# Performance work log

Measured on AMD Instinct MI355X. Metric: run time of the kernel, lower is better.

Reference implementation:

```python
import jax, jax.numpy as jnp
import numpy as np

N, R, D, T, H, MM, OBJ, PLN = 1024, 100, 256, 14, 8, 600, 36, 16
DH = D // H


def _plin(w, x):
    # monotone piecewise-linear map on [0,1] with PLN segments (Counter's PiecewiseLin)
    w = jnp.abs(w).at[0].set(0.0)
    w = w / w.sum()
    cs = jnp.cumsum(w)  # knot values, cs[PLN] == 1
    y = PLN * jnp.clip(x, 0.0, 1.0)
    i = jnp.clip(jnp.floor(y).astype(jnp.int32), 0, PLN)
    f = y - jnp.floor(y)
    return cs[i] + f * w[jnp.clip(i + 1, 0, PLN)]


def _iou(b):
    # b: (N, m, 4) as x1,y1,x2,y2 -> pairwise IoU (N, m, m)
    area = jnp.clip(b[..., 2] - b[..., 0], 0.0) * jnp.clip(b[..., 3] - b[..., 1], 0.0)
    lt = jnp.maximum(b[:, :, None, :2], b[:, None, :, :2])
    rb = jnp.minimum(b[:, :, None, 2:], b[:, None, :, 2:])
    wh = jnp.clip(rb - lt, 0.0)
    inter = wh[..., 0] * wh[..., 1]
    return inter / (area[:, :, None] + area[:, None, :] - inter + 1e-12)


def _counter(boxes, att, pw):
    # Zhang et al. counting module, already_sigmoided=True
    att_top, idx = jax.lax.top_k(att, OBJ)                       # (N, m)
    btop = jnp.take_along_axis(boxes, idx[:, :, None], axis=1)   # (N, m, 4)
    rel = att_top[:, :, None] * att_top[:, None, :]              # outer product of attention
    dist = 1.0 - _iou(btop)
    score = _plin(pw[0], rel) * _plin(pw[1], dist)
    dscore = _plin(pw[3], rel) * _plin(pw[4], dist)
    # deduplication via outer differences
    att_diff = jnp.abs(att_top[:, :, None] - att_top[:, None, :])
    sd = jnp.abs(dscore[:, :, :, None] - dscore[:, :, None, :])  # (N, m, m, m)
    sim = jnp.prod(_plin(pw[2], 1.0 - sd), axis=1) * _plin(pw[2], 1.0 - att_diff)
    row_sims = sim.sum(axis=2)                                   # (N, m), >= 1 (diagonal)
    all_sims = row_sims[:, :, None] * row_sims[:, None, :]
    score = score / all_sims
    correction = _plin(pw[0], att_top * att_top) / row_sims
    total = jnp.sqrt(score.sum(axis=(1, 2)) + correction.sum(axis=1) + 1e-20)  # (N,)
    # to_one_hot: soft one-hot between floor and ceil counts
    s = jnp.clip(total, 0.0, float(OBJ))
    i = jnp.clip(jnp.floor(s).astype(jnp.int32), 0, OBJ)
    f = s - jnp.floor(s)
    oh_l = jax.nn.one_hot(i, OBJ + 1, dtype=s.dtype)
    oh_r = jax.nn.one_hot(jnp.clip(i + 1, 0, OBJ), OBJ + 1, dtype=s.dtype)
    one_hot = (1.0 - f)[:, None] * oh_l + f[:, None] * oh_r
    att_conf = jnp.abs(_plin(pw[5], att_top) - 0.5)
    dist_conf = jnp.abs(_plin(pw[6], dist) - 0.5)
    conf = _plin(pw[7], att_conf.mean(axis=1) + dist_conf.mean(axis=(1, 2)))  # (N,)
    return one_hot * conf[:, None], conf


def _layernorm(x, g, b):
    mu = x.mean(-1, keepdims=True)
    var = ((x - mu) ** 2).mean(-1, keepdims=True)
    return (x - mu) / jnp.sqrt(var + 1e-5) * g + b


def setup_inputs():
    key = jax.random.key(0)
    ks = jax.random.split(key, 20)
    lin = lambda k, o, i: jax.random.normal(k, (o, i), dtype=jnp.float32) * 0.02
    z = lambda o: jnp.zeros((o,), jnp.float32)
    v_emb = jax.random.normal(ks[0], (N, R, D), dtype=jnp.float32)
    q_emb = jax.random.normal(ks[1], (N, T, D), dtype=jnp.float32)
    xy = jax.random.uniform(ks[2], (N, R, 2), dtype=jnp.float32) * 0.8
    wh = jax.random.uniform(ks[3], (N, R, 2), dtype=jnp.float32) * 0.19 + 0.01
    boxes = jnp.concatenate([xy, xy + wh], axis=-1)  # valid x1,y1,x2,y2 in [0,1]
    pw = jax.random.uniform(ks[4], (8, PLN + 1), dtype=jnp.float32, minval=0.5, maxval=1.5)
    pw = pw.at[:, 0].set(0.0)
    return {
        'v_emb': v_emb, 'q_emb': q_emb, 'boxes': boxes,
        'Wq': lin(ks[5], D, D), 'bq': z(D),
        'Wk': lin(ks[6], D, D), 'bk': z(D),
        'Wv': lin(ks[7], D, D), 'bv': z(D),
        'in_w': lin(ks[8], 3 * D, D), 'in_b': z(3 * D),
        'out_w': lin(ks[9], D, D), 'out_b': z(D),
        'ln_g': jnp.ones((D,), jnp.float32), 'ln_b': z(D),
        'l0_w': lin(ks[10], MM, D), 'l0_b': z(MM),
        'l1_w': lin(ks[11], MM, D), 'l1_b': z(MM),
        'lo_w': lin(ks[12], 1, MM), 'lo_b': z(1),
        'pw': pw,
    }


def reference(v_emb, q_emb, boxes, Wq, bq, Wk, bk, Wv, bv, in_w, in_b, out_w, out_b,
              ln_g, ln_b, l0_w, l0_b, l1_w, l1_b, lo_w, lo_b, pw):
    n = v_emb.shape[0]
    # pre-projections then nn.MultiheadAttention (eval, no dropout)
    q = v_emb @ Wq.T + bq
    k = v_emb @ Wk.T + bk
    v = v_emb @ Wv.T + bv
    wq, wk, wv = jnp.split(in_w, 3, axis=0)
    biq, bik, biv = jnp.split(in_b, 3)
    qh = (q @ wq.T + biq).reshape(n, R, H, DH)
    kh = (k @ wk.T + bik).reshape(n, R, H, DH)
    vh = (v @ wv.T + biv).reshape(n, R, H, DH)
    logits = jnp.einsum('nqhd,nkhd->nhqk', qh, kh) * (1.0 / np.sqrt(DH))
    attn = jax.nn.softmax(logits, axis=-1)
    ao = jnp.einsum('nhqk,nkhd->nqhd', attn, vh).reshape(n, R, D)
    ao = ao @ out_w.T + out_b
    inter = _layernorm(ao, ln_g, ln_b)
    # MLB bilinear fusion with mean-pooled question, normalize=True, no activations
    q_pool = q_emb.mean(axis=1)                 # (N, D)
    x0 = inter @ l0_w.T + l0_b                  # (N, R, MM)
    x1 = q_pool @ l1_w.T + l1_b                 # (N, MM)
    zf = x0 * x1[:, None, :]
    zf = jnp.sign(zf) * jnp.sqrt(jnp.abs(zf))   # signed sqrt
    zf = zf / jnp.maximum(jnp.linalg.norm(zf, axis=-1, keepdims=True), 1e-12)
    scores = jax.nn.sigmoid(zf @ lo_w.T + lo_b)  # (N, R, 1)
    pred, conf = _counter(boxes, scores[..., 0], pw)
    return scores, pred, conf
```

## Files before the change

### kernel.cpp

```cpp
#include <hip/hip_runtime.h>

#define N_   1024
#define R_   100
#define D_   256
#define T_   14
#define H_   8
#define DH_  32
#define MM_  600
#define OBJ_ 36

typedef _Float16 f16;
typedef __attribute__((ext_vector_type(8))) _Float16 f16x8;
typedef __attribute__((ext_vector_type(4))) _Float16 f16x4v;
typedef __attribute__((ext_vector_type(4))) float f32x4;

__device__ __forceinline__ void f2h_split(float x, f16& hi, f16& lo) {
  hi = (_Float16)x;
  lo = (_Float16)(x - (float)hi);
}

#define GL16(gp, lp) __builtin_amdgcn_global_load_lds( \
    (const __attribute__((address_space(1))) void*)(gp), \
    (__attribute__((address_space(3))) void*)(lp), 16, 0, 0)

__device__ __forceinline__ float plin_f(const float* __restrict__ w,
                                        const float* __restrict__ cs, float x) {
  float xc = fminf(fmaxf(x, 0.f), 1.f);
  float y  = 16.f * xc;
  float fy = floorf(y);
  int   i  = (int)fy;
  float f  = y - fy;
  int   ip = i + 1; if (ip > 16) ip = 16;
  return cs[i] + f * w[ip];
}

__global__ void prep_plin(const float* __restrict__ pw, float* __restrict__ plw,
                          float* __restrict__ plc) {
  int p = threadIdx.x;
  if (p < 8) {
    float w[17];
    float sum = 0.f;
    w[0] = 0.f;
    for (int k = 1; k < 17; ++k) { w[k] = fabsf(pw[p*17 + k]); sum += w[k]; }
    float inv = 1.f / sum;
    float c = 0.f;
    for (int k = 0; k < 17; ++k) {
      float wk = w[k] * inv;
      c += wk;
      plw[p*17 + k] = wk;
      plc[p*17 + k] = c;
    }
  }
}

__global__ void fuse_c(const float* __restrict__ in_w, const float* __restrict__ in_b,
                       const float* __restrict__ bq, const float* __restrict__ bk,
                       const float* __restrict__ bv, float* __restrict__ c) {
  int i = blockIdx.x * blockDim.x + threadIdx.x;
  if (i < 768) {
    const float* bsel = (i < 256) ? bq : ((i < 512) ? bk : bv);
    float acc = in_b[i];
    for (int o = 0; o < 256; ++o) acc += in_w[(size_t)i*256 + o] * bsel[o];
    c[i] = acc;
  }
}

__global__ __launch_bounds__(256) void fuse_A(const float* __restrict__ in_w,
    const float* __restrict__ Wq, const float* __restrict__ Wk,
    const float* __restrict__ Wv, f16* __restrict__ Ahi, f16* __restrict__ Alo) {
  int i = blockIdx.x;
  int j = threadIdx.x;
  const float* Wsel = (i < 256) ? Wq : ((i < 512) ? Wk : Wv);
  __shared__ float row[256];
  row[j] = in_w[(size_t)i*256 + j];
  __syncthreads();
  float acc = 0.f;
  for (int o = 0; o < 256; ++o) acc += row[o] * Wsel[(size_t)o*256 + j];
  f16 h, l; f2h_split(acc, h, l);
  Ahi[(size_t)i*256 + j] = h;
  Alo[(size_t)i*256 + j] = l;
}

__global__ __launch_bounds__(256) void split_vec(const float* __restrict__ in,
    f16* __restrict__ hi, f16* __restrict__ lo, int n4) {
  int i = blockIdx.x * blockDim.x + threadIdx.x;
  if (i < n4) {
    float4 v = ((const float4*)in)[i];
    union { f16 h[4]; ushort4 u; } H, L;
    f2h_split(v.x, H.h[0], L.h[0]);
    f2h_split(v.y, H.h[1], L.h[1]);
    f2h_split(v.z, H.h[2], L.h[2]);
    f2h_split(v.w, H.h[3], L.h[3]);
    ((ushort4*)hi)[i] = H.u;
    ((ushort4*)lo)[i] = L.u;
  }
}

__global__ __launch_bounds__(256) void conv_w600(const float* __restrict__ w,
    f16* __restrict__ hi, f16* __restrict__ lo) {
  int o = blockIdx.x;
  int j = threadIdx.x;
  f16 h = (f16)0.f, l = (f16)0.f;
  if (o < 600) f2h_split(w[(size_t)o*256 + j], h, l);
  hi[(size_t)o*256 + j] = h;
  lo[(size_t)o*256 + j] = l;
}

__global__ __launch_bounds__(256) void pool_split(const float* __restrict__ q_emb,
    f16* __restrict__ qph, f16* __restrict__ qpl) {
  int n = blockIdx.x, tid = threadIdx.x;
  float s = 0.f;
  for (int t = 0; t < 14; ++t) s += q_emb[((size_t)n*14 + t)*256 + tid];
  s *= (1.f/14.f);
  f16 h, l; f2h_split(s, h, l);
  qph[(size_t)n*256 + tid] = h;
  qpl[(size_t)n*256 + tid] = l;
}

template<bool BOUND>
__global__ __launch_bounds__(256) void gemm_f16s(
    const f16* __restrict__ Xhi, const f16* __restrict__ Xlo,
    const f16* __restrict__ Whi, const f16* __restrict__ Wlo,
    const float* __restrict__ bias, float* __restrict__ C, int Oreal) {
  __shared__ f16 XsH[128 * 32];
  __shared__ f16 XsL[128 * 32];
  __shared__ f16 WsH[128 * 32];
  __shared__ f16 WsL[128 * 32];
  const int tid  = threadIdx.x;
  const int wave = tid >> 6, lane = tid & 63;
  const int bm = blockIdx.x * 128, bn = blockIdx.y * 128;
  const int wm = (wave & 1) * 64, wn = (wave >> 1) * 64;
  const int col = lane & 15, quad = lane >> 4;

  const int s = wave * 64 + lane;
  const int r0 = s >> 2,         cseg = (s & 3) * 8;
  const int r1 = (s + 256) >> 2;
  const size_t o0 = (size_t)(bm + r0) * 256 + cseg;
  const size_t o1 = (size_t)(bm + r1) * 256 + cseg;
  const size_t p0 = (size_t)(bn + r0) * 256 + cseg;
  const size_t p1 = (size_t)(bn + r1) * 256 + cseg;
  char* XHB = (char*)XsH + wave * 1024;
  char* XLB = (char*)XsL + wave * 1024;
  char* WHB = (char*)WsH + wave * 1024;
  char* WLB = (char*)WsL + wave * 1024;

  f32x4 acc[4][4] = {};

  for (int k0 = 0; k0 < 256; k0 += 32) {
    GL16(Xhi + o0 + k0, XHB);
    GL16(Xhi + o1 + k0, XHB + 4096);
    GL16(Xlo + o0 + k0, XLB);
    GL16(Xlo + o1 + k0, XLB + 4096);
    GL16(Whi + p0 + k0, WHB);
    GL16(Whi + p1 + k0, WHB + 4096);
    GL16(Wlo + p0 + k0, WLB);
    GL16(Wlo + p1 + k0, WLB + 4096);
    __syncthreads();

    f16x8 ah[4], al[4], bh[4], bl[4];
#pragma unroll
    for (int i = 0; i < 4; ++i) {
      int ro = (wm + i*16 + col) * 32 + quad * 8;
      ah[i] = *(const f16x8*)(XsH + ro);
      al[i] = *(const f16x8*)(XsL + ro);
    }
#pragma unroll
    for (int j = 0; j < 4; ++j) {
      int ro = (wn + j*16 + col) * 32 + quad * 8;
      bh[j] = *(const f16x8*)(WsH + ro);
      bl[j] = *(const f16x8*)(WsL + ro);
    }
#pragma unroll
    for (int i = 0; i < 4; ++i)
#pragma unroll
      for (int j = 0; j < 4; ++j) {
        acc[i][j] = __builtin_amdgcn_mfma_f32_16x16x32_f16(al[i], bh[j], acc[i][j], 0, 0, 0);
        acc[i][j] = __builtin_amdgcn_mfma_f32_16x16x32_f16(ah[i], bl[j], acc[i][j], 0, 0, 0);
        acc[i][j] = __builtin_amdgcn_mfma_f32_16x16x32_f16(ah[i], bh[j], acc[i][j], 0, 0, 0);
      }
    __syncthreads();
  }

#pragma unroll
  for (int j = 0; j < 4; ++j) {
    int o = bn + wn + j*16 + col;
    if (BOUND && o >= Oreal) continue;
    float bo = bias[o];
#pragma unroll
    for (int i = 0; i < 4; ++i) {
#pragma unroll
      for (int r = 0; r < 4; ++r) {
        int m = bm + wm + i*16 + quad*4 + r;
        C[(size_t)m * Oreal + o] = acc[i][j][r] + bo;
      }
    }
  }
}

__global__ __launch_bounds__(256) void gemm2_ln(
    const f16* __restrict__ Xhi, const f16* __restrict__ Xlo,
    const f16* __restrict__ Whi, const f16* __restrict__ Wlo,
    const float* __restrict__ bias, const float* __restrict__ g,
    const float* __restrict__ b, f16* __restrict__ ohi, f16* __restrict__ olo) {
  __shared__ f16 XsH[128 * 32];
  __shared__ f16 XsL[128 * 32];
  __shared__ f16 WsH[256 * 32];
  __shared__ f16 WsL[256 * 32];
  __shared__ float gbb[768];
  const int tid  = threadIdx.x;
  const int wave = tid >> 6, lane = tid & 63;
  const int bm = blockIdx.x * 128;
  const int wm = wave * 32;
  const int col16 = lane & 15, quad = lane >> 4;

  for (int i = tid; i < 768; i += 256)
    gbb[i] = (i < 256) ? g[i] : ((i < 512) ? b[i - 256] : bias[i - 512]);

  const int s = wave * 64 + lane;
  const int rx0 = s >> 2, cseg = (s & 3) * 8;
  const int rx1 = (s + 256) >> 2;
  const size_t o0 = (size_t)(bm + rx0) * 256 + cseg;
  const size_t o1 = (size_t)(bm + rx1) * 256 + cseg;
  char* XHB = (char*)XsH + wave * 1024;
  char* XLB = (char*)XsL + wave * 1024;

  f32x4 acc[2][16] = {};

  for (int k0 = 0; k0 < 256; k0 += 32) {
    GL16(Xhi + o0 + k0, XHB);
    GL16(Xhi + o1 + k0, XHB + 4096);
    GL16(Xlo + o0 + k0, XLB);
    GL16(Xlo + o1 + k0, XLB + 4096);
#pragma unroll
    for (int is = 0; is < 4; ++is) {
      int sw = is * 256 + s;
      size_t wo = (size_t)(sw >> 2) * 256 + (sw & 3) * 8 + k0;
      GL16(Whi + wo, (char*)WsH + is * 4096 + wave * 1024);
      GL16(Wlo + wo, (char*)WsL + is * 4096 + wave * 1024);
    }
    __syncthreads();

    f16x8 ah[2], al[2];
#pragma unroll
    for (int i = 0; i < 2; ++i) {
      int ro = (wm + i*16 + col16) * 32 + quad * 8;
      ah[i] = *(const f16x8*)(XsH + ro);
      al[i] = *(const f16x8*)(XsL + ro);
    }
#pragma unroll
    for (int j = 0; j < 16; ++j) {
      int ro = (j*16 + col16) * 32 + quad * 8;
      f16x8 bh = *(const f16x8*)(WsH + ro);
      f16x8 bl = *(const f16x8*)(WsL + ro);
#pragma unroll
      for (int i = 0; i < 2; ++i) {
        acc[i][j] = __builtin_amdgcn_mfma_f32_16x16x32_f16(al[i], bh, acc[i][j], 0, 0, 0);
        acc[i][j] = __builtin_amdgcn_mfma_f32_16x16x32_f16(ah[i], bl, acc[i][j], 0, 0, 0);
        acc[i][j] = __builtin_amdgcn_mfma_f32_16x16x32_f16(ah[i], bh, acc[i][j], 0, 0, 0);
      }
    }
    __syncthreads();
  }

#pragma unroll
  for (int i = 0; i < 2; ++i) {
#pragma unroll
    for (int r = 0; r < 4; ++r) {
      float x[16];
      float sum = 0.f;
#pragma unroll
      for (int j = 0; j < 16; ++j) {
        float v = acc[i][j][r] + gbb[512 + j*16 + col16];
        x[j] = v;
        sum += v;
      }
#pragma unroll
      for (int msk = 1; msk < 16; msk <<= 1) sum += __shfl_xor(sum, msk, 64);
      float mu = sum * (1.f/256.f);
      float s2 = 0.f;
#pragma unroll
      for (int j = 0; j < 16; ++j) { float d = x[j] - mu; s2 += d * d; }
#pragma unroll
      for (int msk = 1; msk < 16; msk <<= 1) s2 += __shfl_xor(s2, msk, 64);
      float inv = rsqrtf(s2 * (1.f/256.f) + 1e-5f);
      size_t m = (size_t)(bm + wm + i*16 + quad*4 + r);
#pragma unroll
      for (int j = 0; j < 16; ++j) {
        int col = j*16 + col16;
        float yv = (x[j] - mu) * inv * gbb[col] + gbb[256 + col];
        f16 hh, ll; f2h_split(yv, hh, ll);
        ohi[m*256 + col] = hh;
        olo[m*256 + col] = ll;
      }
    }
  }
}

__global__ __launch_bounds__(512) void attn_mfma(const float* __restrict__ qkv,
    f16* __restrict__ aohi, f16* __restrict__ aolo) {
  const int n = blockIdx.x >> 3;
  const int h = blockIdx.x & 7;
  __shared__ f16 KH[112*32], KL[112*32];
  __shared__ f16 VTH[32*116], VTL[32*116];
  __shared__ unsigned int P32[112*116];
  const int tid = threadIdx.x;
  const int wave = tid >> 6, lane = tid & 63;
  const int col16 = lane & 15, quad = lane >> 4;
  const float scale = 0.17677669529663687f;
  const float* base = qkv + (size_t)n * 100 * 768 + h * 32;
  const int tm = wave;

  float qv[8];
  if (tm < 7) {
    int m = tm*16 + col16; if (m > 99) m = 99;
    const float* qp = base + (size_t)m * 768 + quad*8;
    float4 q0 = *(const float4*)(qp);
    float4 q1 = *(const float4*)(qp + 4);
    qv[0]=q0.x; qv[1]=q0.y; qv[2]=q0.z; qv[3]=q0.w;
    qv[4]=q1.x; qv[5]=q1.y; qv[6]=q1.z; qv[7]=q1.w;
  } else {
#pragma unroll
    for (int j = 0; j < 8; ++j) qv[j] = 0.f;
  }

  for (int idx = tid; idx < 112*32; idx += 512) {
    int r = idx >> 5, d = idx & 31;
    float kv = 0.f, vv = 0.f;
    if (r < 100) {
      const float* p = base + (size_t)r * 768;
      kv = p[256 + d];
      vv = p[512 + d];
    }
    f16 khh, kll, vhh, vll;
    f2h_split(kv, khh, kll);
    f2h_split(vv, vhh, vll);
    KH[idx] = khh; KL[idx] = kll;
    VTH[d*116 + r] = vhh; VTL[d*116 + r] = vll;
  }
  __syncthreads();

  if (tm < 7) {
    f16x8 ah, al;
#pragma unroll
    for (int j = 0; j < 8; ++j) {
      f16 hh, ll; f2h_split(qv[j] * scale, hh, ll); ah[j] = hh; al[j] = ll;
    }
    f32x4 sacc[7];
#pragma unroll
    for (int tn = 0; tn < 7; ++tn) {
      int off = (tn*16 + col16)*32 + quad*8;
      f16x8 bh = *(const f16x8*)(KH + off);
      f16x8 bl = *(const f16x8*)(KL + off);
      f32x4 a = {};
      a = __builtin_amdgcn_mfma_f32_16x16x32_f16(al, bh, a, 0, 0, 0);
      a = __builtin_amdgcn_mfma_f32_16x16x32_f16(ah, bl, a, 0, 0, 0);
      a = __builtin_amdgcn_mfma_f32_16x16x32_f16(ah, bh, a, 0, 0, 0);
      sacc[tn] = a;
    }
    if (col16 >= 4) {
      sacc[6][0] = -1e30f; sacc[6][1] = -1e30f;
      sacc[6][2] = -1e30f; sacc[6][3] = -1e30f;
    }
    float mx[4];
#pragma unroll
    for (int r = 0; r < 4; ++r) {
      float mv = sacc[0][r];
#pragma unroll
      for (int tn = 1; tn < 7; ++tn) mv = fmaxf(mv, sacc[tn][r]);
      mx[r] = mv;
    }
#pragma unroll
    for (int msk = 1; msk < 16; msk <<= 1)
#pragma unroll
      for (int r = 0; r < 4; ++r) mx[r] = fmaxf(mx[r], __shfl_xor(mx[r], msk, 64));
    float sm[4] = {0.f, 0.f, 0.f, 0.f};
#pragma unroll
    for (int tn = 0; tn < 7; ++tn)
#pragma unroll
      for (int r = 0; r < 4; ++r) {
        float p = __expf(sacc[tn][r] - mx[r]);
        sacc[tn][r] = p;
        sm[r] += p;
      }
#pragma unroll
    for (int msk = 1; msk < 16; msk <<= 1)
#pragma unroll
      for (int r = 0; r < 4; ++r) sm[r] += __shfl_xor(sm[r], msk, 64);
    float inv[4];
#pragma unroll
    for (int r = 0; r < 4; ++r) inv[r] = 1.f / sm[r];
#pragma unroll
    for (int tn = 0; tn < 7; ++tn)
#pragma unroll
      for (int r = 0; r < 4; ++r) {
        float p = sacc[tn][r] * inv[r];
        f16 hh, ll; f2h_split(p, hh, ll);
        union { struct { f16 h, l; } f; unsigned int u; } pk;
        pk.f.h = hh; pk.f.l = ll;
        P32[(tm*16 + quad*4 + r)*116 + tn*16 + col16] = pk.u;
      }

    f16x8 vh[2][4], vl[2][4];
#pragma unroll
    for (int td = 0; td < 2; ++td)
#pragma unroll
      for (int kc = 0; kc < 4; ++kc) {
        if (kc == 3 && quad >= 2) {
          f16x8 z = {};
          vh[td][kc] = z; vl[td][kc] = z;
        } else {
          int off = (td*16 + col16)*116 + kc*32 + quad*8;
          f16x4v h0 = *(const f16x4v*)(VTH + off);
          f16x4v h1 = *(const f16x4v*)(VTH + off + 4);
          f16x4v l0 = *(const f16x4v*)(VTL + off);
          f16x4v l1 = *(const f16x4v*)(VTL + off + 4);
          f16x8 hv, lv;
#pragma unroll
          for (int t = 0; t < 4; ++t) { hv[t] = h0[t]; hv[t+4] = h1[t]; lv[t] = l0[t]; lv[t+4] = l1[t]; }
          vh[td][kc] = hv; vl[td][kc] = lv;
        }
      }
    f32x4 acc[2] = {};
#pragma unroll
    for (int kc = 0; kc < 4; ++kc) {
      f16x8 ph, pl;
      if (kc == 3 && quad >= 2) {
        f16x8 z = {};
        ph = z; pl = z;
      } else {
        const unsigned int* pp = P32 + (tm*16 + col16)*116 + kc*32 + quad*8;
        f16x8 e0 = *(const f16x8*)(pp);
        f16x8 e1 = *(const f16x8*)(pp + 4);
        ph = __builtin_shufflevector(e0, e1, 0, 2, 4, 6, 8, 10, 12, 14);
        pl = __builtin_shufflevector(e0, e1, 1, 3, 5, 7, 9, 11, 13, 15);
      }
#pragma unroll
      for (int td = 0; td < 2; ++td) {
        acc[td] = __builtin_amdgcn_mfma_f32_16x16x32_f16(pl, vh[td][kc], acc[td], 0, 0, 0);
        acc[td] = __builtin_amdgcn_mfma_f32_16x16x32_f16(ph, vl[td][kc], acc[td], 0, 0, 0);
        acc[td] = __builtin_amdgcn_mfma_f32_16x16x32_f16(ph, vh[td][kc], acc[td], 0, 0, 0);
      }
    }
#pragma unroll
    for (int td = 0; td < 2; ++td) {
#pragma unroll
      for (int r = 0; r < 4; ++r) {
        int m = tm*16 + quad*4 + r;
        if (m < 100) {
          size_t oidx = ((size_t)n*100 + m)*256 + h*32 + td*16 + col16;
          f16 hh, ll; f2h_split(acc[td][r], hh, ll);
          aohi[oidx] = hh;
          aolo[oidx] = ll;
        }
      }
    }
  }
}

__global__ __launch_bounds__(256) void mlb_kernel(const float* __restrict__ x0,
    const float* __restrict__ x1, const float* __restrict__ lo_w,
    const float* __restrict__ lo_b, float* __restrict__ out) {
  const int wave = threadIdx.x >> 6, lane = threadIdx.x & 63;
  const size_t m = (size_t)blockIdx.x * 4 + wave;
  const size_t n = m / 100;
  const float* xr = x0 + m * 600;
  const float* yr = x1 + n * 600;
  float ss = 0.f, dot = 0.f;
  for (int e = lane; e < 600; e += 64) {
    float v = xr[e] * yr[e];
    float r = (v >= 0.f) ? sqrtf(v) : -sqrtf(-v);
    ss  += r * r;
    dot += r * lo_w[e];
  }
#pragma unroll
  for (int o = 32; o > 0; o >>= 1) {
    ss  += __shfl_xor(ss, o, 64);
    dot += __shfl_xor(dot, o, 64);
  }
  if (lane == 0) {
    float inv = 1.f / fmaxf(sqrtf(ss), 1e-12f);
    float sc = dot * inv + lo_b[0];
    out[m] = 1.f / (1.f + __expf(-sc));
  }
}

__device__ __forceinline__ float breduce(float v, float* red, int tid) {
  for (int o = 32; o > 0; o >>= 1) v += __shfl_down(v, o, 64);
  if ((tid & 63) == 0) red[tid >> 6] = v;
  __syncthreads();
  float r = red[0] + red[1] + red[2] + red[3];
  __syncthreads();
  return r;
}

__global__ __launch_bounds__(256) void counter_kernel(
    const float* __restrict__ scores, const float* __restrict__ boxes,
    const float* __restrict__ plw, const float* __restrict__ plc,
    float* __restrict__ pred, float* __restrict__ conf_out) {
  int n = blockIdx.x, tid = threadIdx.x;
  __shared__ float plw_s[8][17], plc_s[8][17];
  __shared__ float sval[128];
  __shared__ int   sidx[128];
  __shared__ float att[36], bx[36][4];
  __shared__ float dist[36][36], scr[36][36], ds2[36][36], sim[36][36];
  __shared__ float rs[36];
  __shared__ float red[4];
  __shared__ float b_f, b_cf;
  __shared__ int   b_i;

  for (int i = tid; i < 136; i += 256) {
    (&plw_s[0][0])[i] = plw[i];
    (&plc_s[0][0])[i] = plc[i];
  }
  if (tid < 128) {
    sval[tid] = (tid < 100) ? scores[(size_t)n*100 + tid] : -1e30f;
    sidx[tid] = tid;
  }
  __syncthreads();

  for (int k = 2; k <= 128; k <<= 1) {
    for (int j = k >> 1; j > 0; j >>= 1) {
      if (tid < 128) {
        int ixj = tid ^ j;
        if (ixj > tid) {
          float va = sval[tid], vb = sval[ixj];
          int   ia = sidx[tid], ib = sidx[ixj];
          bool a_before_b = (va > vb) || (va == vb && ia < ib);
          bool ascending = ((tid & k) == 0);
          bool doswap = ascending ? !a_before_b : a_before_b;
          if (doswap) { sval[tid] = vb; sval[ixj] = va; sidx[tid] = ib; sidx[ixj] = ia; }
        }
      }
      __syncthreads();
    }
  }

  if (tid < 36) {
    att[tid] = sval[tid];
    const float* bp = boxes + ((size_t)n*100 + sidx[tid])*4;
    bx[tid][0] = bp[0]; bx[tid][1] = bp[1]; bx[tid][2] = bp[2]; bx[tid][3] = bp[3];
  }
  __syncthreads();

  for (int idx = tid; idx < 1296; idx += 256) {
    int i = idx / 36, j = idx % 36;
    float x1a = bx[i][0], y1a = bx[i][1], x2a = bx[i][2], y2a = bx[i][3];
    float x1b = bx[j][0], y1b = bx[j][1], x2b = bx[j][2], y2b = bx[j][3];
    float areaA = fmaxf(x2a - x1a, 0.f) * fmaxf(y2a - y1a, 0.f);
    float areaB = fmaxf(x2b - x1b, 0.f) * fmaxf(y2b - y1b, 0.f);
    float iw = fmaxf(fminf(x2a, x2b) - fmaxf(x1a, x1b), 0.f);
    float ih = fmaxf(fminf(y2a, y2b) - fmaxf(y1a, y1b), 0.f);
    float inter = iw * ih;
    float iou = inter / (areaA + areaB - inter + 1e-12f);
    float dd = 1.f - iou;
    float rel = att[i] * att[j];
    dist[i][j] = dd;
    scr[i][j]  = plin_f(plw_s[0], plc_s[0], rel) * plin_f(plw_s[1], plc_s[1], dd);
    ds2[i][j]  = plin_f(plw_s[3], plc_s[3], rel) * plin_f(plw_s[4], plc_s[4], dd);
  }
  __syncthreads();

  for (int idx = tid; idx < 1296; idx += 256) {
    int b = idx / 36, c = idx % 36;
    float p = plin_f(plw_s[2], plc_s[2], 1.f - fabsf(att[b] - att[c]));
    for (int a = 0; a < 36; ++a)
      p *= plin_f(plw_s[2], plc_s[2], 1.f - fabsf(ds2[a][b] - ds2[a][c]));
    sim[b][c] = p;
  }
  __syncthreads();

  if (tid < 36) {
    float s = 0.f;
    for (int c = 0; c < 36; ++c) s += sim[tid][c];
    rs[tid] = s;
  }
  __syncthreads();

  float p1 = 0.f, p4 = 0.f;
  for (int idx = tid; idx < 1296; idx += 256) {
    int b = idx / 36, c = idx % 36;
    p1 += scr[b][c] / (rs[b] * rs[c]);
    p4 += fabsf(plin_f(plw_s[6], plc_s[6], dist[b][c]) - 0.5f);
  }
  float p2 = 0.f, p3 = 0.f;
  if (tid < 36) {
    p2 = plin_f(plw_s[0], plc_s[0], att[tid]*att[tid]) / rs[tid];
    p3 = fabsf(plin_f(plw_s[5], plc_s[5], att[tid]) - 0.5f);
  }
  float s1 = breduce(p1, red, tid);
  float s2 = breduce(p2, red, tid);
  float s3 = breduce(p3, red, tid);
  float s4 = breduce(p4, red, tid);

  if (tid == 0) {
    float total = sqrtf(s1 + s2 + 1e-20f);
    float cf = plin_f(plw_s[7], plc_s[7], s3 * (1.f/36.f) + s4 * (1.f/1296.f));
    float sc = fminf(fmaxf(total, 0.f), 36.f);
    float fl = floorf(sc);
    int ii = (int)fl; if (ii > 36) ii = 36;
    b_f = sc - fl;
    b_i = ii;
    b_cf = cf;
    conf_out[n] = cf;
  }
  __syncthreads();
  if (tid < 37) {
    int ii = b_i;
    int ir = (ii + 1 > 36) ? 36 : ii + 1;
    float v = ((tid == ii) ? (1.f - b_f) : 0.f) + ((tid == ir) ? b_f : 0.f);
    pred[(size_t)n*37 + tid] = v * b_cf;
  }
}

extern "C" void kernel_launch(void* const* d_in, const int* in_sizes, int n_in,
                              void* d_out, int out_size, void* d_ws, size_t ws_size,
                              hipStream_t stream) {
  const float* v_emb = (const float*)d_in[0];
  const float* q_emb = (const float*)d_in[1];
  const float* boxes = (const float*)d_in[2];
  const float* Wq    = (const float*)d_in[3];
  const float* bq    = (const float*)d_in[4];
  const float* Wk    = (const float*)d_in[5];
  const float* bk    = (const float*)d_in[6];
  const float* Wv    = (const float*)d_in[7];
  const float* bv    = (const float*)d_in[8];
  const float* in_w  = (const float*)d_in[9];
  const float* in_b  = (const float*)d_in[10];
  const float* out_w = (const float*)d_in[11];
  const float* out_b = (const float*)d_in[12];
  const float* ln_g  = (const float*)d_in[13];
  const float* ln_b  = (const float*)d_in[14];
  const float* l0_w  = (const float*)d_in[15];
  const float* l0_b  = (const float*)d_in[16];
  const float* l1_w  = (const float*)d_in[17];
  const float* l1_b  = (const float*)d_in[18];
  const float* lo_w  = (const float*)d_in[19];
  const float* lo_b  = (const float*)d_in[20];
  const float* pw    = (const float*)d_in[21];

  float* ws = (float*)d_ws;
  float* plw   = ws + 0;
  float* plc   = ws + 256;
  float* cbuf  = ws + 512;
  float* x1    = ws + 1280;
  f16* hb = (f16*)(ws + 615680);
  f16* A_hi    = hb + 0;
  f16* A_lo    = hb + 196608;
  f16* outw_hi = hb + 393216;
  f16* outw_lo = hb + 458752;
  f16* l0w_hi  = hb + 524288;
  f16* l0w_lo  = hb + 688128;
  f16* l1w_hi  = hb + 851968;
  f16* l1w_lo  = hb + 1015808;
  f16* qp_hi   = hb + 1179648;
  f16* qp_lo   = hb + 1441792;
  f16* v_hi    = hb + 1703936;
  f16* v_lo    = hb + 27918336;
  const size_t small_floats = 615680 + 27066368;

  size_t avail = (ws_size / 4 > small_floats) ? (ws_size / 4 - small_floats) : 0;
  int NC = 1024;
  while (NC > 32 && (size_t)NC * 188000ull > avail) NC >>= 1;

  float* qkv_c = ws + small_floats;
  float* x0_c  = qkv_c + (size_t)NC * 76800;
  f16* ao_hi  = (f16*)(x0_c + (size_t)NC * 60000);
  f16* ao_lo  = ao_hi + (size_t)NC * 25600;
  f16* int_hi = ao_lo + (size_t)NC * 25600;
  f16* int_lo = int_hi + (size_t)NC * 25600;

  float* out    = (float*)d_out;
  float* scores = out;
  float* pred   = out + 102400;
  float* conf   = out + 140288;

  prep_plin<<<1, 64, 0, stream>>>(pw, plw, plc);
  fuse_c<<<3, 256, 0, stream>>>(in_w, in_b, bq, bk, bv, cbuf);
  fuse_A<<<768, 256, 0, stream>>>(in_w, Wq, Wk, Wv, A_hi, A_lo);
  split_vec<<<(65536/4 + 255)/256, 256, 0, stream>>>(out_w, outw_hi, outw_lo, 65536/4);
  conv_w600<<<640, 256, 0, stream>>>(l0_w, l0w_hi, l0w_lo);
  conv_w600<<<640, 256, 0, stream>>>(l1_w, l1w_hi, l1w_lo);
  split_vec<<<(26214400/4 + 255)/256, 256, 0, stream>>>(v_emb, v_hi, v_lo, 26214400/4);
  pool_split<<<N_, 256, 0, stream>>>(q_emb, qp_hi, qp_lo);
  {
    dim3 gx(1024/128, 5);
    gemm_f16s<true><<<gx, 256, 0, stream>>>(qp_hi, qp_lo, l1w_hi, l1w_lo,
                                            l1_b, x1, 600);
  }

  for (int n0 = 0; n0 < N_; n0 += NC) {
    const int M = NC * 100;
    const size_t voff = (size_t)n0 * 100 * 256;

    dim3 g1(M / 128, 6);
    gemm_f16s<false><<<g1, 256, 0, stream>>>(v_hi + voff, v_lo + voff,
                                             A_hi, A_lo, cbuf, qkv_c, 768);

    attn_mfma<<<NC * H_, 512, 0, stream>>>(qkv_c, ao_hi, ao_lo);

    gemm2_ln<<<M / 128, 256, 0, stream>>>(ao_hi, ao_lo, outw_hi, outw_lo,
                                          out_b, ln_g, ln_b, int_hi, int_lo);

    dim3 g3(M / 128, 5);
    gemm_f16s<true><<<g3, 256, 0, stream>>>(int_hi, int_lo, l0w_hi, l0w_lo,
                                            l0_b, x0_c, 600);

    mlb_kernel<<<M / 4, 256, 0, stream>>>(x0_c, x1 + (size_t)n0 * 600, lo_w, lo_b,
                                          scores + (size_t)n0 * 100);
  }

  counter_kernel<<<N_, 256, 0, stream>>>(scores, boxes, plw, plc, pred, conf);
}
```

Measured before the change: 988.9 us.

## Fuse MLB signed-sqrt/norm/dot epilogue into l0 GEMM with partial sums

Replaces the l0 GEMM that wrote the full x0 activation (M x 600 floats) plus a separate MLB kernel with a GEMM whose epilogue computes the signed sqrt, the squared norm and the lo_w dot product per row tile. It writes per-tile partial sums, which a small reduce kernel combines into the sigmoid scores. This removes the large x0 write and re-read, and the smaller workspace allows bigger chunks. In exchange it adds shuffle reductions and per-element x1 loads in the epilogue, plus a second small launch.

Measured after the change: 995.6 us. No clear change (+0.7%).

```diff
diff --git a/kernel.cpp b/kernel.cpp
--- a/kernel.cpp
+++ b/kernel.cpp
@@ -197,6 +197,121 @@
   }
 }
 
+__global__ __launch_bounds__(256) void gemm_l0_mlb(
+    const f16* __restrict__ Xhi, const f16* __restrict__ Xlo,
+    const f16* __restrict__ Whi, const f16* __restrict__ Wlo,
+    const float* __restrict__ bias, const float* __restrict__ x1,
+    const float* __restrict__ lo_w, float2* __restrict__ part) {
+  __shared__ f16 XsH[128 * 32];
+  __shared__ f16 XsL[128 * 32];
+  __shared__ f16 WsH[128 * 32];
+  __shared__ f16 WsL[128 * 32];
+  const int tid  = threadIdx.x;
+  const int wave = tid >> 6, lane = tid & 63;
+  const int bm = blockIdx.x * 128, bn = blockIdx.y * 128;
+  const int wm = (wave & 1) * 64, wn = (wave >> 1) * 64;
+  const int col = lane & 15, quad = lane >> 4;
+
+  const int s = wave * 64 + lane;
+  const int r0 = s >> 2,         cseg = (s & 3) * 8;
+  const int r1 = (s + 256) >> 2;
+  const size_t o0 = (size_t)(bm + r0) * 256 + cseg;
+  const size_t o1 = (size_t)(bm + r1) * 256 + cseg;
+  const size_t p0 = (size_t)(bn + r0) * 256 + cseg;
+  const size_t p1 = (size_t)(bn + r1) * 256 + cseg;
+  char* XHB = (char*)XsH + wave * 1024;
+  char* XLB = (char*)XsL + wave * 1024;
+  char* WHB = (char*)WsH + wave * 1024;
+  char* WLB = (char*)WsL + wave * 1024;
+
+  f32x4 acc[4][4] = {};
+
+  for (int k0 = 0; k0 < 256; k0 += 32) {
+    GL16(Xhi + o0 + k0, XHB);
+    GL16(Xhi + o1 + k0, XHB + 4096);
+    GL16(Xlo + o0 + k0, XLB);
+    GL16(Xlo + o1 + k0, XLB + 4096);
+    GL16(Whi + p0 + k0, WHB);
+    GL16(Whi + p1 + k0, WHB + 4096);
+    GL16(Wlo + p0 + k0, WLB);
+    GL16(Wlo + p1 + k0, WLB + 4096);
+    __syncthreads();
+
+    f16x8 ah[4], al[4], bh[4], bl[4];
+#pragma unroll
+    for (int i = 0; i < 4; ++i) {
+      int ro = (wm + i*16 + col) * 32 + quad * 8;
+      ah[i] = *(const f16x8*)(XsH + ro);
+      al[i] = *(const f16x8*)(XsL + ro);
+    }
+#pragma unroll
+    for (int j = 0; j < 4; ++j) {
+      int ro = (wn + j*16 + col) * 32 + quad * 8;
+      bh[j] = *(const f16x8*)(WsH + ro);
+      bl[j] = *(const f16x8*)(WsL + ro);
+    }
+#pragma unroll
+    for (int i = 0; i < 4; ++i)
+#pragma unroll
+      for (int j = 0; j < 4; ++j) {
+        acc[i][j] = __builtin_amdgcn_mfma_f32_16x16x32_f16(al[i], bh[j], acc[i][j], 0, 0, 0);
+        acc[i][j] = __builtin_amdgcn_mfma_f32_16x16x32_f16(ah[i], bl[j], acc[i][j], 0, 0, 0);
+        acc[i][j] = __builtin_amdgcn_mfma_f32_16x16x32_f16(ah[i], bh[j], acc[i][j], 0, 0, 0);
+      }
+    __syncthreads();
+  }
+
+  float bo[4], lw[4];
+#pragma unroll
+  for (int j = 0; j < 4; ++j) {
+    int o = bn + wn + j*16 + col;
+    bo[j] = (o < 600) ? bias[o] : 0.f;
+    lw[j] = (o < 600) ? lo_w[o] : 0.f;
+  }
+#pragma unroll
+  for (int i = 0; i < 4; ++i) {
+#pragma unroll
+    for (int rr = 0; rr < 4; ++rr) {
+      int m = bm + wm + i*16 + quad*4 + rr;
+      int nimg = m / 100;
+      const float* x1r = x1 + (size_t)nimg * 600;
+      float ss = 0.f, dt = 0.f;
+#pragma unroll
+      for (int j = 0; j < 4; ++j) {
+        int o = bn + wn + j*16 + col;
+        if (o < 600) {
+          float v = (acc[i][j][rr] + bo[j]) * x1r[o];
+          float rt = (v >= 0.f) ? sqrtf(v) : -sqrtf(-v);
+          ss += rt * rt;
+          dt += rt * lw[j];
+        }
+      }
+#pragma unroll
+      for (int msk = 1; msk < 16; msk <<= 1) {
+        ss += __shfl_xor(ss, msk, 64);
+        dt += __shfl_xor(dt, msk, 64);
+      }
+      if (col == 0) {
+        float2 pv; pv.x = ss; pv.y = dt;
+        part[(size_t)m * 10 + blockIdx.y * 2 + (wn >> 6)] = pv;
+      }
+    }
+  }
+}
+
+__global__ __launch_bounds__(256) void mlb_reduce(const float2* __restrict__ part,
+    const float* __restrict__ lo_b, float* __restrict__ out, int M) {
+  int m = blockIdx.x * 256 + threadIdx.x;
+  if (m < M) {
+    const float2* p = part + (size_t)m * 10;
+    float ss = 0.f, dt = 0.f;
+#pragma unroll
+    for (int t = 0; t < 10; ++t) { float2 v = p[t]; ss += v.x; dt += v.y; }
+    float sc = dt / fmaxf(sqrtf(ss), 1e-12f) + lo_b[0];
+    out[m] = 1.f / (1.f + __expf(-sc));
+  }
+}
+
 __global__ __launch_bounds__(256) void gemm2_ln(
     const f16* __restrict__ Xhi, const f16* __restrict__ Xlo,
     const f16* __restrict__ Whi, const f16* __restrict__ Wlo,
@@ -454,33 +569,6 @@
         }
       }
     }
-  }
-}
-
-__global__ __launch_bounds__(256) void mlb_kernel(const float* __restrict__ x0,
-    const float* __restrict__ x1, const float* __restrict__ lo_w,
-    const float* __restrict__ lo_b, float* __restrict__ out) {
-  const int wave = threadIdx.x >> 6, lane = threadIdx.x & 63;
-  const size_t m = (size_t)blockIdx.x * 4 + wave;
-  const size_t n = m / 100;
-  const float* xr = x0 + m * 600;
-  const float* yr = x1 + n * 600;
-  float ss = 0.f, dot = 0.f;
-  for (int e = lane; e < 600; e += 64) {
-    float v = xr[e] * yr[e];
-    float r = (v >= 0.f) ? sqrtf(v) : -sqrtf(-v);
-    ss  += r * r;
-    dot += r * lo_w[e];
-  }
-#pragma unroll
-  for (int o = 32; o > 0; o >>= 1) {
-    ss  += __shfl_xor(ss, o, 64);
-    dot += __shfl_xor(dot, o, 64);
-  }
-  if (lane == 0) {
-    float inv = 1.f / fmaxf(sqrtf(ss), 1e-12f);
-    float sc = dot * inv + lo_b[0];
-    out[m] = 1.f / (1.f + __expf(-sc));
   }
 }
 
@@ -660,11 +748,11 @@
 
   size_t avail = (ws_size / 4 > small_floats) ? (ws_size / 4 - small_floats) : 0;
   int NC = 1024;
-  while (NC > 32 && (size_t)NC * 188000ull > avail) NC >>= 1;
+  while (NC > 32 && (size_t)NC * 130000ull > avail) NC >>= 1;
 
   float* qkv_c = ws + small_floats;
-  float* x0_c  = qkv_c + (size_t)NC * 76800;
-  f16* ao_hi  = (f16*)(x0_c + (size_t)NC * 60000);
+  float2* part = (float2*)(qkv_c + (size_t)NC * 76800);
+  f16* ao_hi  = (f16*)((float*)(void*)part + (size_t)NC * 2000);
   f16* ao_lo  = ao_hi + (size_t)NC * 25600;
   f16* int_hi = ao_lo + (size_t)NC * 25600;
   f16* int_lo = int_hi + (size_t)NC * 25600;
@@ -702,11 +790,11 @@
                                           out_b, ln_g, ln_b, int_hi, int_lo);
 
     dim3 g3(M / 128, 5);
-    gemm_f16s<true><<<g3, 256, 0, stream>>>(int_hi, int_lo, l0w_hi, l0w_lo,
-                                            l0_b, x0_c, 600);
-
-    mlb_kernel<<<M / 4, 256, 0, stream>>>(x0_c, x1 + (size_t)n0 * 600, lo_w, lo_b,
-                                          scores + (size_t)n0 * 100);
+    gemm_l0_mlb<<<g3, 256, 0, stream>>>(int_hi, int_lo, l0w_hi, l0w_lo,
+                                        l0_b, x1 + (size_t)n0 * 600, lo_w, part);
+
+    mlb_reduce<<<(M + 255)/256, 256, 0, stream>>>(part, lo_b,
+                                                  scores + (size_t)n0 * 100, M);
   }
 
   counter_kernel<<<N_, 256, 0, stream>>>(scores, boxes, plw, plc, pred, conf);
```
